# Kernel tuning notes

Hardware: AMD Instinct MI355X
Metric: run time of the kernel (lower is better)

## Reference

```python
import jax, jax.numpy as jnp
import numpy as np

N_NODES = 4096
D_FEAT = 256


def _interp_linear_2x(x):
    # Matches F.interpolate(mode='linear', scale_factor=2, align_corners=False)
    # applied along the node axis. x: [N, D] -> [2N, D]
    n = x.shape[0]
    out_i = jnp.arange(2 * n, dtype=jnp.float32)
    src = jnp.clip((out_i + 0.5) * 0.5 - 0.5, 0.0, float(n - 1))
    i0 = jnp.floor(src).astype(jnp.int32)
    i1 = jnp.minimum(i0 + 1, n - 1)
    w = (src - i0.astype(jnp.float32))[:, None]
    return x[i0] * (1.0 - w) + x[i1] * w


def _nearest_neighbor_idx(x):
    # argmin over pairwise Euclidean distances with diagonal excluded.
    # Squared distances give the same argmin as torch.cdist.
    sq = jnp.sum(x * x, axis=1)
    d2 = sq[:, None] + sq[None, :] - 2.0 * (x @ x.T)  # [2N, 2N]
    m = x.shape[0]
    d2 = jnp.where(jnp.eye(m, dtype=bool), jnp.inf, d2)
    return jnp.argmin(d2, axis=1)


def setup_inputs() -> dict:
    key = jax.random.key(0)
    k1, k2, k3, k4 = jax.random.split(key, 4)
    x = jax.random.normal(k1, (N_NODES, D_FEAT), dtype=jnp.float32)
    adj = jax.random.uniform(k2, (N_NODES, N_NODES), dtype=jnp.float32)
    # Xavier-uniform-ish init for the two GCN weights
    lim = float(np.sqrt(6.0 / (D_FEAT + D_FEAT)))
    W1 = jax.random.uniform(k3, (D_FEAT, D_FEAT), jnp.float32, -lim, lim)
    W2 = jax.random.uniform(k4, (D_FEAT, D_FEAT), jnp.float32, -lim, lim)
    return {"x": x, "adj": adj, "W1": W1, "W2": W2}


def reference(x, adj, W1, W2):
    # conv1: adj @ (x @ W1)
    h = adj @ (x @ W1)                      # [N, D]
    x2 = _interp_linear_2x(h)               # [2N, D]
    # nearest-neighbor one-hot adjacency, then conv2.
    # one_hot(nn_idx) @ support == support[nn_idx] (exact same math)
    nn_idx = _nearest_neighbor_idx(x2)      # [2N]
    support = x2 @ W2                       # [2N, D]
    return support[nn_idx]                  # [2N, D]
```

## Files before the change

kernel.cpp:

```cpp
#include <hip/hip_runtime.h>
#include <hip/hip_bf16.h>
#include <cstdint>

typedef __attribute__((ext_vector_type(8))) __bf16 bf16x8;
typedef __attribute__((ext_vector_type(4))) float f32x4;

static __device__ __forceinline__ unsigned short f2bf(float f) {
  return __builtin_bit_cast(unsigned short, (__bf16)f);
}
static __device__ __forceinline__ unsigned pack2(float a, float b) {
  return (unsigned)f2bf(a) | ((unsigned)f2bf(b) << 16);
}
#define GLDS(src, dst) __builtin_amdgcn_global_load_lds( \
    (const __attribute__((address_space(1))) void*)(src), \
    (__attribute__((address_space(3))) void*)(dst), 16, 0, 0)


__global__ void transpose_w_kernel(const float* __restrict__ W1, const float* __restrict__ W2,
                                   unsigned short* __restrict__ W1t, unsigned short* __restrict__ W2t) {
  int i = blockIdx.x * 256 + threadIdx.x;
  int k = i >> 8, n = i & 255;
  W1t[n * 256 + k] = f2bf(W1[k * 256 + n]);
  W2t[n * 256 + k] = f2bf(W2[k * 256 + n]);
}

__global__ void upsample_kernel(const unsigned short* __restrict__ hs,
                                unsigned short* __restrict__ x2b, float* __restrict__ sq) {
  int row = blockIdx.x * 4 + (threadIdx.x >> 6);
  int c = (threadIdx.x & 63) * 4;
  float s = (row + 0.5f) * 0.5f - 0.5f;
  s = fminf(fmaxf(s, 0.0f), 4095.0f);
  float fl = floorf(s);
  int i0 = (int)fl;
  int i1 = min((int)fl + 1, 4095);
  float w = s - fl;
  float v0[4] = {0.f, 0.f, 0.f, 0.f}, v1[4] = {0.f, 0.f, 0.f, 0.f};
  #pragma unroll
  for (int k = 0; k < 8; ++k) {
    ushort4 u0 = *(const ushort4*)&hs[(size_t)k * 4096 * 256 + i0 * 256 + c];
    ushort4 u1 = *(const ushort4*)&hs[(size_t)k * 4096 * 256 + i1 * 256 + c];
    v0[0] += __builtin_bit_cast(float, (unsigned)u0.x << 16);
    v0[1] += __builtin_bit_cast(float, (unsigned)u0.y << 16);
    v0[2] += __builtin_bit_cast(float, (unsigned)u0.z << 16);
    v0[3] += __builtin_bit_cast(float, (unsigned)u0.w << 16);
    v1[0] += __builtin_bit_cast(float, (unsigned)u1.x << 16);
    v1[1] += __builtin_bit_cast(float, (unsigned)u1.y << 16);
    v1[2] += __builtin_bit_cast(float, (unsigned)u1.z << 16);
    v1[3] += __builtin_bit_cast(float, (unsigned)u1.w << 16);
  }
  float p = 0.f;
  ushort4 st;
  unsigned short* sp = (unsigned short*)&st;
  #pragma unroll
  for (int e = 0; e < 4; ++e) {
    float v = v0[e] * (1.0f - w) + v1[e] * w;
    sp[e] = f2bf(v);
    p += v * v;
  }
  *(ushort4*)&x2b[(size_t)row * 256 + c] = st;
  #pragma unroll
  for (int m = 32; m > 0; m >>= 1) p += __shfl_down(p, m, 64);
  if ((threadIdx.x & 63) == 0) sq[row] = p;
}

__global__ void argmin_reduce_kernel(const unsigned* __restrict__ pv,
                                     unsigned* __restrict__ pck) {
  int row = blockIdx.x * 256 + threadIdx.x;
  int cr = row >> 7;
  unsigned best = 0xFFFFFFFFu;
  for (int c = 0; c <= cr; ++c) best = min(best, pv[(size_t)c * 8192 + row]);
  for (int c = cr + 1; c < 64; ++c) best = min(best, pv[(size_t)(64 + c) * 8192 + row]);
  pck[row] = best & 0x1FFFu;
}

__launch_bounds__(256)
__global__ void adj_gemm_kernel(const float* __restrict__ adjp,
                                const unsigned short* __restrict__ Ttp,
                                unsigned short* __restrict__ hs) {
  constexpr int NT = 8;
  __shared__ alignas(16) unsigned short As[2][64 * 64];
  __shared__ alignas(16) unsigned short Bs[2][256 * 64];

  const int tid = threadIdx.x;
  const int wid = tid >> 6;
  const int lane = tid & 63;
  const int g = lane >> 4, lr = lane & 15;
  const int m0 = blockIdx.x * 64;
  const int kbase = blockIdx.y * 512;
  unsigned short* outp = hs + (size_t)blockIdx.y * 4096 * 256;

  const int srow = tid >> 3;
  const int scp = tid & 7;
  const int ssc = scp ^ (srow & 7);
  const float* aBase0 = adjp + (size_t)(m0 + srow) * 4096 + kbase + ssc * 8;
  const float* aBase1 = aBase0 + (size_t)32 * 4096;
  const unsigned short* bBase = Ttp + (size_t)srow * 4096 + kbase + ssc * 8;

  f32x4 acc[4][4];
  const f32x4 fzero = {0.f, 0.f, 0.f, 0.f};
  #pragma unroll
  for (int i = 0; i < 4; ++i)
    #pragma unroll
    for (int j = 0; j < 4; ++j) acc[i][j] = fzero;

  float4 ar[2][2];
  auto loadA = [&](int t) {
    #pragma unroll
    for (int it = 0; it < 2; ++it) {
      const float* s = (it ? aBase1 : aBase0) + t * 64;
      ar[it][0] = *(const float4*)s;
      ar[it][1] = *(const float4*)(s + 4);
    }
  };
  auto writeA = [&](int buf) {
    #pragma unroll
    for (int it = 0; it < 2; ++it) {
      uint4 pk = { pack2(ar[it][0].x, ar[it][0].y), pack2(ar[it][0].z, ar[it][0].w),
                   pack2(ar[it][1].x, ar[it][1].y), pack2(ar[it][1].z, ar[it][1].w) };
      *(uint4*)&As[buf][(it * 32 + srow) * 64 + scp * 8] = pk;
    }
  };
  auto stageB = [&](int t, int buf) {
    #pragma unroll
    for (int it = 0; it < 8; ++it)
      GLDS(bBase + (size_t)it * 32 * 4096 + t * 64, Bs[buf] + ((size_t)it * 256 + wid * 64) * 8);
  };

  loadA(0);
  stageB(0, 0);
  writeA(0);

  #pragma unroll
  for (int t = 0; t < NT; ++t) {
    const int cur = t & 1;
    if (t + 1 < NT) {
      loadA(t + 1);
      stageB(t + 1, cur ^ 1);
      asm volatile("s_waitcnt vmcnt(12) lgkmcnt(0)" ::: "memory");
    } else {
      asm volatile("s_waitcnt vmcnt(0) lgkmcnt(0)" ::: "memory");
    }
    __builtin_amdgcn_sched_barrier(0);
    __builtin_amdgcn_s_barrier();
    __builtin_amdgcn_sched_barrier(0);
    #pragma unroll
    for (int kk = 0; kk < 2; ++kk) {
      const int ch = (kk * 4 + g) ^ (lr & 7);
      bf16x8 a[4], b[4];
      #pragma unroll
      for (int i = 0; i < 4; ++i)
        a[i] = *(const bf16x8*)&As[cur][(i * 16 + lr) * 64 + ch * 8];
      #pragma unroll
      for (int j = 0; j < 4; ++j)
        b[j] = *(const bf16x8*)&Bs[cur][(wid * 64 + j * 16 + lr) * 64 + ch * 8];
      #pragma unroll
      for (int i = 0; i < 4; ++i)
        #pragma unroll
        for (int j = 0; j < 4; ++j)
          acc[i][j] = __builtin_amdgcn_mfma_f32_16x16x32_bf16(a[i], b[j], acc[i][j], 0, 0, 0);
    }
    __builtin_amdgcn_s_barrier();
    if (t + 1 < NT) writeA(cur ^ 1);
  }

  #pragma unroll
  for (int i = 0; i < 4; ++i) {
    int mrow = m0 + i * 16 + g * 4;
    #pragma unroll
    for (int j = 0; j < 4; ++j) {
      int col = wid * 64 + j * 16 + lr;
      #pragma unroll
      for (int r = 0; r < 4; ++r)
        outp[(size_t)(mrow + r) * 256 + col] = f2bf(acc[i][j][r]);
    }
  }
}

__launch_bounds__(256, 3)
__global__ void gram_kernel(const unsigned short* __restrict__ X,
                            const float* __restrict__ sq,
                            unsigned* __restrict__ pv) {
  __shared__ alignas(16) unsigned short As[128 * 64];
  __shared__ alignas(16) unsigned short Bs[128 * 64];
  __shared__ unsigned mrgr[2][128];
  __shared__ unsigned mrgc[2][128];

  const int tid = threadIdx.x;
  const int wid = tid >> 6;
  const int lane = tid & 63;
  const int g = lane >> 4, lr = lane & 15;
  const int wr = wid >> 1, wc = wid & 1;

  int t = blockIdx.x;
  int bi = (int)((sqrtf(8.0f * (float)t + 1.0f) - 1.0f) * 0.5f);
  while ((bi + 1) * (bi + 2) / 2 <= t) ++bi;
  while (bi * (bi + 1) / 2 > t) --bi;
  const int bx = bi;
  const int by = t - bi * (bi + 1) / 2;
  const int m0 = bx * 128;
  const int n0 = by * 128;
  const bool diag = (bx == by);

  const int srow = tid >> 3;
  const int ssc = (tid & 7) ^ (srow & 7);
  const unsigned short* aBase = X + (size_t)(m0 + srow) * 256 + ssc * 8;
  const unsigned short* bBase = X + (size_t)(n0 + srow) * 256 + ssc * 8;
  unsigned short* const aDst = As + (size_t)(tid >> 6) * 512;
  unsigned short* const bDst = Bs + (size_t)(tid >> 6) * 512;
  const unsigned short* const Bsrc = diag ? As : Bs;

  f32x4 acc[4][4];
  const f32x4 fzero = {0.f, 0.f, 0.f, 0.f};
  #pragma unroll
  for (int i = 0; i < 4; ++i)
    #pragma unroll
    for (int j = 0; j < 4; ++j) acc[i][j] = fzero;

  #pragma unroll
  for (int ks = 0; ks < 4; ++ks) {
    #pragma unroll
    for (int it = 0; it < 4; ++it)
      GLDS(aBase + it * 8192 + ks * 64, aDst + it * 2048);
    if (!diag) {
      #pragma unroll
      for (int it = 0; it < 4; ++it)
        GLDS(bBase + it * 8192 + ks * 64, bDst + it * 2048);
    }
    __syncthreads();
    #pragma unroll
    for (int kk = 0; kk < 2; ++kk) {
      const int ch = (kk * 4 + g) ^ (lr & 7);
      bf16x8 b[4];
      #pragma unroll
      for (int j = 0; j < 4; ++j)
        b[j] = *(const bf16x8*)&Bsrc[(wc * 64 + j * 16 + lr) * 64 + ch * 8];
      #pragma unroll
      for (int i = 0; i < 4; ++i) {
        bf16x8 a = *(const bf16x8*)&As[(wr * 64 + i * 16 + lr) * 64 + ch * 8];
        #pragma unroll
        for (int j = 0; j < 4; ++j)
          acc[i][j] = __builtin_amdgcn_mfma_f32_16x16x32_bf16(a, b[j], acc[i][j], 0, 0, 0);
      }
    }
    __syncthreads();
  }

  int jcol[4];
  float sqj[4];
  unsigned ckey[4];
  #pragma unroll
  for (int j = 0; j < 4; ++j) {
    jcol[j] = n0 + wc * 64 + j * 16 + lr;
    sqj[j] = sq[jcol[j]];
    ckey[j] = 0xFFFFFFFFu;
  }
  #pragma unroll
  for (int i = 0; i < 4; ++i) {
    #pragma unroll
    for (int r = 0; r < 4; ++r) {
      const int lrow = wr * 64 + i * 16 + g * 4 + r;
      const int irow = m0 + lrow;
      const float sqi = sq[irow];
      unsigned rk = 0xFFFFFFFFu;
      #pragma unroll
      for (int j = 0; j < 4; ++j) {
        float v = fmaf(-2.0f, acc[i][j][r], sqi + sqj[j]);
        unsigned bits = __float_as_uint(v) & 0xFFFFE000u;
        unsigned krow = bits | (unsigned)jcol[j];
        if (diag && jcol[j] == irow) krow = 0xFFFFFFFFu;
        rk = min(rk, krow);
        if (!diag) ckey[j] = min(ckey[j], bits | (unsigned)irow);
      }
      #pragma unroll
      for (int m = 1; m < 16; m <<= 1)
        rk = min(rk, (unsigned)__shfl_xor((int)rk, m, 64));
      if (lr == 0) mrgr[wc][lrow] = rk;
    }
  }
  if (!diag) {
    #pragma unroll
    for (int j = 0; j < 4; ++j) {
      ckey[j] = min(ckey[j], (unsigned)__shfl_xor((int)ckey[j], 16, 64));
      ckey[j] = min(ckey[j], (unsigned)__shfl_xor((int)ckey[j], 32, 64));
      if (g == 0) mrgc[wr][wc * 64 + j * 16 + lr] = ckey[j];
    }
  }
  __syncthreads();
  if (tid < 128) {
    pv[(size_t)by * 8192 + m0 + tid] = min(mrgr[0][tid], mrgr[1][tid]);
  } else if (!diag) {
    int c = tid - 128;
    pv[(size_t)(64 + bx) * 8192 + n0 + c] = min(mrgc[0][c], mrgc[1][c]);
  }
}

template <int BM, int BN, int WAVES_M, int KT, int EPI, bool AF32, bool GATHER>
__launch_bounds__(256)
__global__ void gemm_nt_kernel(const void* __restrict__ Ap, int lda,
                               const unsigned short* __restrict__ Bp, int ldb,
                               int M, int N,
                               float* __restrict__ Cf,
                               unsigned short* __restrict__ Cb,
                               const unsigned* __restrict__ gidx) {
  constexpr int BK = 64;
  constexpr int NT = KT / BK;
  constexpr int WAVES_N = 4 / WAVES_M;
  constexpr int WM = BM / WAVES_M;
  constexpr int WN = BN / WAVES_N;
  constexpr int FM = WM / 16;
  constexpr int FN = WN / 16;
  constexpr int ASLOT = BM * 8;
  constexpr int AITER = (ASLOT + 255) / 256;
  constexpr int BITER = (BN * 8) / 256;

  __shared__ alignas(16) unsigned short As[BM * BK];
  __shared__ alignas(16) unsigned short Bs[BN * BK];

  const int tid = threadIdx.x;
  const int wid = tid >> 6;
  const int lane = tid & 63;
  const int g = lane >> 4;
  const int lr = lane & 15;
  const int wr = wid / WAVES_N;
  const int wc = wid % WAVES_N;
  const int m0 = blockIdx.x * BM;
  const int n0 = blockIdx.y * BN;
  constexpr int kbase = 0;

  const int srow = tid >> 3;
  const int ssc = (tid & 7) ^ (srow & 7);
  const float* aBF[AITER];
  const unsigned short* aBH[AITER];
  #pragma unroll
  for (int it = 0; it < AITER; ++it) {
    int r = m0 + srow + it * 32;
    if constexpr (AF32) {
      aBF[it] = (const float*)Ap + (size_t)r * (size_t)lda + kbase + ssc * 8;
    } else {
      int sr = GATHER ? (int)gidx[r] : r;
      aBH[it] = (const unsigned short*)Ap + (size_t)sr * (size_t)lda + kbase + ssc * 8;
    }
  }
  const unsigned short* bBase = Bp + (size_t)(n0 + srow) * (size_t)ldb + kbase + ssc * 8;
  unsigned short* const sDst = As + (size_t)wid * 512;
  unsigned short* const bDst = Bs + (size_t)wid * 512;

  f32x4 acc[FM][FN];
  const f32x4 fzero = {0.f, 0.f, 0.f, 0.f};
  #pragma unroll
  for (int i = 0; i < FM; ++i)
    #pragma unroll
    for (int j = 0; j < FN; ++j) acc[i][j] = fzero;

  #pragma unroll
  for (int t = 0; t < NT; ++t) {
    #pragma unroll
    for (int it = 0; it < BITER; ++it)
      GLDS(bBase + (size_t)it * 32 * ldb + t * 64, bDst + it * 2048);
    if constexpr (AF32) {
      #pragma unroll
      for (int it = 0; it < AITER; ++it) {
        if (ASLOT % 256 == 0 || it * 256 + tid < ASLOT) {
          const float* src = aBF[it] + t * 64;
          float4 f0 = *(const float4*)src;
          float4 f1 = *(const float4*)(src + 4);
          uint4 pk = { pack2(f0.x, f0.y), pack2(f0.z, f0.w),
                       pack2(f1.x, f1.y), pack2(f1.z, f1.w) };
          *(uint4*)&As[(it * 32 + srow) * BK + (tid & 7) * 8] = pk;
        }
      }
    } else {
      #pragma unroll
      for (int it = 0; it < AITER; ++it)
        GLDS(aBH[it] + t * 64, sDst + it * 2048);
    }
    __syncthreads();
    #pragma unroll
    for (int kk = 0; kk < 2; ++kk) {
      const int ch = (kk * 4 + g) ^ (lr & 7);
      bf16x8 a[FM], b[FN];
      #pragma unroll
      for (int i = 0; i < FM; ++i)
        a[i] = *(const bf16x8*)&As[(wr * WM + i * 16 + lr) * BK + ch * 8];
      #pragma unroll
      for (int j = 0; j < FN; ++j)
        b[j] = *(const bf16x8*)&Bs[(wc * WN + j * 16 + lr) * BK + ch * 8];
      #pragma unroll
      for (int i = 0; i < FM; ++i)
        #pragma unroll
        for (int j = 0; j < FN; ++j)
          acc[i][j] = __builtin_amdgcn_mfma_f32_16x16x32_bf16(a[i], b[j], acc[i][j], 0, 0, 0);
    }
    __syncthreads();
  }

  const int rowb = wr * WM;
  const int colb = wc * WN;
  if constexpr (EPI == 0) {
    #pragma unroll
    for (int i = 0; i < FM; ++i) {
      int mrow = m0 + rowb + i * 16 + g * 4;
      #pragma unroll
      for (int j = 0; j < FN; ++j) {
        int col = n0 + colb + j * 16 + lr;
        #pragma unroll
        for (int r = 0; r < 4; ++r)
          Cf[(size_t)(mrow + r) * N + col] = acc[i][j][r];
      }
    }
  } else {
    #pragma unroll
    for (int i = 0; i < FM; ++i) {
      int mrow = m0 + rowb + i * 16 + g * 4;
      #pragma unroll
      for (int j = 0; j < FN; ++j) {
        int col = n0 + colb + j * 16 + lr;
        ushort4 st;
        st.x = f2bf(acc[i][j][0]);
        st.y = f2bf(acc[i][j][1]);
        st.z = f2bf(acc[i][j][2]);
        st.w = f2bf(acc[i][j][3]);
        *(ushort4*)&Cb[(size_t)col * M + mrow] = st;
      }
    }
  }
}


extern "C" void kernel_launch(void* const* d_in, const int* in_sizes, int n_in,
                              void* d_out, int out_size, void* d_ws, size_t ws_size,
                              hipStream_t stream) {
  (void)in_sizes; (void)n_in; (void)out_size; (void)ws_size;
  const float* x   = (const float*)d_in[0];
  const float* adj = (const float*)d_in[1];
  const float* W1  = (const float*)d_in[2];
  const float* W2  = (const float*)d_in[3];
  float* out = (float*)d_out;

  char* p = (char*)d_ws;
  unsigned short* Tt  = (unsigned short*)p;  p += 4096 * 256 * 2;
  char* R             = p;                   p += 16 * 1024 * 1024;
  unsigned short* x2b = (unsigned short*)p;  p += 8192 * 256 * 2;
  float* sqv          = (float*)p;           p += 8192 * 4;
  unsigned* pck       = (unsigned*)p;        p += 8192 * 4;
  unsigned short* W1t = (unsigned short*)p;  p += 256 * 256 * 2;
  unsigned short* W2t = (unsigned short*)p;  p += 256 * 256 * 2;

  unsigned short* hs = (unsigned short*)R;
  unsigned* pv       = (unsigned*)R;

  transpose_w_kernel<<<256, 256, 0, stream>>>(W1, W2, W1t, W2t);

  gemm_nt_kernel<64, 64, 4, 256, 1, true, false><<<dim3(64, 4), 256, 0, stream>>>(
      x, 256, W1t, 256, 4096, 256, nullptr, Tt, nullptr);

  adj_gemm_kernel<<<dim3(64, 8), 256, 0, stream>>>(adj, Tt, hs);

  upsample_kernel<<<2048, 256, 0, stream>>>(hs, x2b, sqv);

  gram_kernel<<<2080, 256, 0, stream>>>(x2b, sqv, pv);

  argmin_reduce_kernel<<<32, 256, 0, stream>>>(pv, pck);

  gemm_nt_kernel<64, 64, 4, 256, 0, false, true><<<dim3(128, 4), 256, 0, stream>>>(
      x2b, 256, W2t, 256, 8192, 256, out, nullptr, pck);
}
```

Baseline: 98.19 us.

## Fuse argmin reduction into gather GEMM and halve adj split-K factor

```diff
diff --git a/kernel.cpp b/kernel.cpp
--- a/kernel.cpp
+++ b/kernel.cpp
@@ -36,7 +36,7 @@
   float w = s - fl;
   float v0[4] = {0.f, 0.f, 0.f, 0.f}, v1[4] = {0.f, 0.f, 0.f, 0.f};
   #pragma unroll
-  for (int k = 0; k < 8; ++k) {
+  for (int k = 0; k < 4; ++k) {
     ushort4 u0 = *(const ushort4*)&hs[(size_t)k * 4096 * 256 + i0 * 256 + c];
     ushort4 u1 = *(const ushort4*)&hs[(size_t)k * 4096 * 256 + i1 * 256 + c];
     v0[0] += __builtin_bit_cast(float, (unsigned)u0.x << 16);
@@ -63,21 +63,11 @@
   if ((threadIdx.x & 63) == 0) sq[row] = p;
 }
 
-__global__ void argmin_reduce_kernel(const unsigned* __restrict__ pv,
-                                     unsigned* __restrict__ pck) {
-  int row = blockIdx.x * 256 + threadIdx.x;
-  int cr = row >> 7;
-  unsigned best = 0xFFFFFFFFu;
-  for (int c = 0; c <= cr; ++c) best = min(best, pv[(size_t)c * 8192 + row]);
-  for (int c = cr + 1; c < 64; ++c) best = min(best, pv[(size_t)(64 + c) * 8192 + row]);
-  pck[row] = best & 0x1FFFu;
-}
-
 __launch_bounds__(256)
 __global__ void adj_gemm_kernel(const float* __restrict__ adjp,
                                 const unsigned short* __restrict__ Ttp,
                                 unsigned short* __restrict__ hs) {
-  constexpr int NT = 8;
+  constexpr int NT = 16;
   __shared__ alignas(16) unsigned short As[2][64 * 64];
   __shared__ alignas(16) unsigned short Bs[2][256 * 64];
 
@@ -86,7 +76,7 @@
   const int lane = tid & 63;
   const int g = lane >> 4, lr = lane & 15;
   const int m0 = blockIdx.x * 64;
-  const int kbase = blockIdx.y * 512;
+  const int kbase = blockIdx.y * 1024;
   unsigned short* outp = hs + (size_t)blockIdx.y * 4096 * 256;
 
   const int srow = tid >> 3;
@@ -301,7 +291,7 @@
                                int M, int N,
                                float* __restrict__ Cf,
                                unsigned short* __restrict__ Cb,
-                               const unsigned* __restrict__ gidx) {
+                               const unsigned* __restrict__ pv) {
   constexpr int BK = 64;
   constexpr int NT = KT / BK;
   constexpr int WAVES_N = 4 / WAVES_M;
@@ -315,6 +305,8 @@
 
   __shared__ alignas(16) unsigned short As[BM * BK];
   __shared__ alignas(16) unsigned short Bs[BN * BK];
+  __shared__ unsigned redp[GATHER ? 4 * 64 : 1];
+  __shared__ unsigned pckl[GATHER ? 64 : 1];
 
   const int tid = threadIdx.x;
   const int wid = tid >> 6;
@@ -325,7 +317,26 @@
   const int wc = wid % WAVES_N;
   const int m0 = blockIdx.x * BM;
   const int n0 = blockIdx.y * BN;
-  constexpr int kbase = 0;
+
+  if constexpr (GATHER) {
+    static_assert(!GATHER || BM == 64, "inline reduce assumes BM==64");
+    const int row = tid & 63;
+    const int part = tid >> 6;
+    const int cr = m0 >> 7;
+    unsigned best = 0xFFFFFFFFu;
+    #pragma unroll
+    for (int s8 = 0; s8 < 16; ++s8) {
+      int s = part * 16 + s8;
+      int slot = s + (s > cr ? 64 : 0);
+      best = min(best, pv[(size_t)slot * 8192 + m0 + row]);
+    }
+    redp[part * 64 + row] = best;
+    __syncthreads();
+    if (tid < 64)
+      pckl[tid] = min(min(redp[tid], redp[64 + tid]),
+                      min(redp[128 + tid], redp[192 + tid])) & 0x1FFFu;
+    __syncthreads();
+  }
 
   const int srow = tid >> 3;
   const int ssc = (tid & 7) ^ (srow & 7);
@@ -335,13 +346,13 @@
   for (int it = 0; it < AITER; ++it) {
     int r = m0 + srow + it * 32;
     if constexpr (AF32) {
-      aBF[it] = (const float*)Ap + (size_t)r * (size_t)lda + kbase + ssc * 8;
+      aBF[it] = (const float*)Ap + (size_t)r * (size_t)lda + ssc * 8;
     } else {
-      int sr = GATHER ? (int)gidx[r] : r;
-      aBH[it] = (const unsigned short*)Ap + (size_t)sr * (size_t)lda + kbase + ssc * 8;
-    }
-  }
-  const unsigned short* bBase = Bp + (size_t)(n0 + srow) * (size_t)ldb + kbase + ssc * 8;
+      int sr = GATHER ? (int)pckl[srow + it * 32] : r;
+      aBH[it] = (const unsigned short*)Ap + (size_t)sr * (size_t)lda + ssc * 8;
+    }
+  }
+  const unsigned short* bBase = Bp + (size_t)(n0 + srow) * (size_t)ldb + ssc * 8;
   unsigned short* const sDst = As + (size_t)wid * 512;
   unsigned short* const bDst = Bs + (size_t)wid * 512;
 
@@ -439,10 +450,9 @@
 
   char* p = (char*)d_ws;
   unsigned short* Tt  = (unsigned short*)p;  p += 4096 * 256 * 2;
-  char* R             = p;                   p += 16 * 1024 * 1024;
+  char* R             = p;                   p += 8 * 1024 * 1024;
   unsigned short* x2b = (unsigned short*)p;  p += 8192 * 256 * 2;
   float* sqv          = (float*)p;           p += 8192 * 4;
-  unsigned* pck       = (unsigned*)p;        p += 8192 * 4;
   unsigned short* W1t = (unsigned short*)p;  p += 256 * 256 * 2;
   unsigned short* W2t = (unsigned short*)p;  p += 256 * 256 * 2;
 
@@ -454,14 +464,12 @@
   gemm_nt_kernel<64, 64, 4, 256, 1, true, false><<<dim3(64, 4), 256, 0, stream>>>(
       x, 256, W1t, 256, 4096, 256, nullptr, Tt, nullptr);
 
-  adj_gemm_kernel<<<dim3(64, 8), 256, 0, stream>>>(adj, Tt, hs);
+  adj_gemm_kernel<<<dim3(64, 4), 256, 0, stream>>>(adj, Tt, hs);
 
   upsample_kernel<<<2048, 256, 0, stream>>>(hs, x2b, sqv);
 
   gram_kernel<<<2080, 256, 0, stream>>>(x2b, sqv, pv);
 
-  argmin_reduce_kernel<<<32, 256, 0, stream>>>(pv, pck);
-
   gemm_nt_kernel<64, 64, 4, 256, 0, false, true><<<dim3(128, 4), 256, 0, stream>>>(
-      x2b, 256, W2t, 256, 8192, 256, out, nullptr, pck);
-}
+      x2b, 256, W2t, 256, 8192, 256, out, nullptr, pv);
+}
```

Measured after the change: 88.83 us. 9.5% less time.
